# Performance work log

Measured on AMD Instinct MI355X. Metric: run time of the kernel, lower is better.

## Reference

```python
import jax, jax.numpy as jnp
import numpy as np

NUM_PHRASE = 8
HDIM = 256
NUM_HEADS = 8
NUM_LAYERS = 3
MIN_DIST = 2


def sine_pos(mask, num_feats, temperature=10000.0):
    # PositionEmbeddingSine (1D, DETR-style, normalize=False)
    B, L = mask.shape
    x_embed = jnp.cumsum(mask.astype(jnp.float32), axis=1)            # [B,L]
    dim_t = jnp.arange(num_feats, dtype=jnp.float32)
    dim_t = temperature ** (2.0 * jnp.floor(dim_t / 2.0) / num_feats)
    pos = x_embed[:, :, None] / dim_t                                  # [B,L,C]
    pos = jnp.stack([jnp.sin(pos[:, :, 0::2]), jnp.cos(pos[:, :, 1::2])], axis=3)
    return pos.reshape(B, L, num_feats)


def layer_norm(x, g, b, eps=1e-5):
    mu = jnp.mean(x, axis=-1, keepdims=True)
    var = jnp.mean((x - mu) ** 2, axis=-1, keepdims=True)
    return (x - mu) / jnp.sqrt(var + eps) * g + b


def mha(q, k, v, key_mask, in_w, in_b, out_w, out_b, nheads):
    # torch nn.MultiheadAttention (batch_first, eval/no-dropout), averaged attn weights
    B, Lq, C = q.shape
    Dh = C // nheads
    qp = (q @ in_w[:, :C] + in_b[:C]).reshape(B, Lq, nheads, Dh)
    kp = (k @ in_w[:, C:2 * C] + in_b[C:2 * C]).reshape(B, -1, nheads, Dh)
    vp = (v @ in_w[:, 2 * C:] + in_b[2 * C:]).reshape(B, -1, nheads, Dh)
    scores = jnp.einsum('bqhd,bkhd->bhqk', qp, kp) / jnp.sqrt(jnp.float32(Dh))
    scores = jnp.where(key_mask[:, None, None, :], scores, -jnp.inf)
    attn = jax.nn.softmax(scores, axis=-1)
    out = jnp.einsum('bhqk,bkhd->bqhd', attn, vp).reshape(B, Lq, C)
    return out @ out_w + out_b, jnp.mean(attn, axis=1)


def cross_attention(x, y, mask, qw, qb, kvw, kvb, inw, inb, ow, ob, g0, b0, lw, lb, g1, b1):
    C = x.shape[-1]
    q = x @ qw + qb
    kv = y @ kvw + kvb
    k, v = kv[..., :C], kv[..., C:]
    q_att, attn = mha(q, k, v, mask, inw, inb, ow, ob, NUM_HEADS)
    x = layer_norm(x + q_att, g0, b0)
    update = jax.nn.relu(x @ lw + lb)
    x = layer_norm(x + update, g1, b1)
    return x, attn


def _select_one(entropy_b, mask_b):
    # greedy highest-entropy selection with min-distance suppression (1D NMS)
    P, MD = NUM_PHRASE, MIN_DIST
    score = jnp.where(mask_b, entropy_b, -jnp.inf)
    order = jnp.argsort(-score).astype(jnp.int32)   # valid indices first, descending entropy

    def step(carry, idx):
        sel, cnt = carry
        dists = jnp.where(sel >= 0, jnp.abs(idx - sel), 1000000)
        ok = mask_b[idx] & (cnt < P) & (jnp.min(dists) >= MD)
        new_sel = jnp.where(ok, sel.at[jnp.minimum(cnt, P - 1)].set(idx), sel)
        return (new_sel, cnt + ok.astype(jnp.int32)), None

    init = (jnp.full((P,), -1, jnp.int32), jnp.int32(0))
    (sel, cnt), _ = jax.lax.scan(step, init, order)
    last = sel[jnp.maximum(cnt - 1, 0)]
    return jnp.where(jnp.arange(P) < cnt, sel, last)   # pad by repeating last


def phrase_generate(txt_emb, txt_mask, video_feats, video_mask,
                    word_proj_w, word_proj_b, video_proj_w, video_proj_b,
                    q_w, q_b, kv_w, kv_b, in_w, in_b, out_w, out_b,
                    ln0_g, ln0_b, lin_w, lin_b, ln1_g, ln1_b, eos_slot):
    B, L, C = txt_emb.shape
    word_emb = txt_emb[:, 1:]
    word_mask = txt_mask[:, 1:]
    word_pe = word_emb + sine_pos(word_mask, C)

    # word importance via video cross-attention entropy
    wp = word_pe @ word_proj_w + word_proj_b                      # [B,Lw,C]
    vp = video_feats @ video_proj_w + video_proj_b                # [B,T,C]
    sim = jnp.einsum('blc,btc->blt', wp, vp)                      # [B,Lw,T]
    sim = jnp.where(video_mask[:, None, :], sim, -jnp.inf)
    attn_weights = jax.nn.softmax(sim, axis=2)
    entropy = -jnp.sum(attn_weights * jnp.log(attn_weights + 1e-6), axis=2)  # [B,Lw]

    sel = jax.vmap(_select_one)(entropy, word_mask)               # [B,P] int32
    phrase_slot = jnp.take_along_axis(word_pe, sel[:, :, None], axis=1)      # [B,P,C]

    slot_sim = None
    for i in range(NUM_LAYERS):
        phrase_slot, slot_sim = cross_attention(
            phrase_slot, word_pe, word_mask,
            q_w[i], q_b[i], kv_w[i], kv_b[i], in_w[i], in_b[i], out_w[i], out_b[i],
            ln0_g[i], ln0_b[i], lin_w[i], lin_b[i], ln1_g[i], ln1_b[i])

    eos = jnp.broadcast_to(eos_slot, (B, 1, C))
    return phrase_slot, attn_weights, slot_sim, eos


def setup_inputs() -> dict:
    key = jax.random.key(0)
    ks = jax.random.split(key, 16)
    B, L, T, C, NL = 128, 257, 1024, HDIM, NUM_LAYERS
    s = 0.02
    inp = {
        'txt_emb': jax.random.normal(ks[0], (B, L, C), jnp.float32),
        'txt_mask': jnp.ones((B, L), jnp.bool_),
        'video_feats': jax.random.normal(ks[1], (B, T, C), jnp.float32),
        'video_mask': jnp.ones((B, T), jnp.bool_),
        'word_proj_w': jax.random.normal(ks[2], (C, C)) * s,
        'word_proj_b': jnp.zeros((C,)),
        'video_proj_w': jax.random.normal(ks[3], (C, C)) * s,
        'video_proj_b': jnp.zeros((C,)),
        'q_w': jax.random.normal(ks[4], (NL, C, C)) * s,
        'q_b': jnp.zeros((NL, C)),
        'kv_w': jax.random.normal(ks[5], (NL, C, 2 * C)) * s,
        'kv_b': jnp.zeros((NL, 2 * C)),
        'in_w': jax.random.normal(ks[6], (NL, C, 3 * C)) * s,
        'in_b': jnp.zeros((NL, 3 * C)),
        'out_w': jax.random.normal(ks[7], (NL, C, C)) * s,
        'out_b': jnp.zeros((NL, C)),
        'ln0_g': jnp.ones((NL, C)),
        'ln0_b': jnp.zeros((NL, C)),
        'lin_w': jax.random.normal(ks[8], (NL, C, C)) * s,
        'lin_b': jnp.zeros((NL, C)),
        'ln1_g': jnp.ones((NL, C)),
        'ln1_b': jnp.zeros((NL, C)),
        'eos_slot': jax.random.normal(ks[9], (1, 1, C)),
    }
    return inp


def reference(txt_emb, txt_mask, video_feats, video_mask,
              word_proj_w, word_proj_b, video_proj_w, video_proj_b,
              q_w, q_b, kv_w, kv_b, in_w, in_b, out_w, out_b,
              ln0_g, ln0_b, lin_w, lin_b, ln1_g, ln1_b, eos_slot):
    return phrase_generate(txt_emb, txt_mask, video_feats, video_mask,
                           word_proj_w, word_proj_b, video_proj_w, video_proj_b,
                           q_w, q_b, kv_w, kv_b, in_w, in_b, out_w, out_b,
                           ln0_g, ln0_b, lin_w, lin_b, ln1_g, ln1_b, eos_slot)
```

## Files before the change

kernel.cpp:

```cpp
#include <hip/hip_runtime.h>
#include <math.h>

#define BB 128
#define LFULL 257
#define LW 256
#define TT 1024
#define CC 256
#define NH 8
#define DHD 32
#define PP 8
#define NLAY 3

typedef __bf16 bf16x8 __attribute__((ext_vector_type(8)));
typedef __bf16 bf16x4 __attribute__((ext_vector_type(4)));
typedef float  f32x4  __attribute__((ext_vector_type(4)));

__device__ __forceinline__ float blockReduceSum(float v, volatile float* lds) {
#pragma unroll
    for (int m = 32; m >= 1; m >>= 1) v += __shfl_xor(v, m);
    __syncthreads();
    if ((threadIdx.x & 63) == 0) lds[threadIdx.x >> 6] = v;
    __syncthreads();
    return lds[0] + lds[1] + lds[2] + lds[3];
}
__device__ __forceinline__ float blockReduceMax(float v, volatile float* lds) {
#pragma unroll
    for (int m = 32; m >= 1; m >>= 1) v = fmaxf(v, __shfl_xor(v, m));
    __syncthreads();
    if ((threadIdx.x & 63) == 0) lds[threadIdx.x >> 6] = v;
    __syncthreads();
    return fmaxf(fmaxf(lds[0], lds[1]), fmaxf(lds[2], lds[3]));
}


__device__ __forceinline__ int ldsoff(int row, int col) {
    return ((row >> 6) << 11)
         + ((((row >> 4) & 3) << 2) + (col >> 3)) * 128
         + ((row & 15) << 3) + (col & 7);
}

template<int SPLIT, int B_F32, int OUT_SPLIT>
__global__ __launch_bounds__(512, 4) void gemm_mfma(
    const __bf16* __restrict__ Ahi, const __bf16* __restrict__ Alo, int lda, long long sA,
    const void* __restrict__ Bhp, const void* __restrict__ Blp, int ldb, long long sB,
    const float* __restrict__ bias,
    float* __restrict__ Cf, __bf16* __restrict__ Chi, __bf16* __restrict__ Clo,
    int ldc, long long sC, int M, int N, int K)
{
    __shared__ __bf16 sAh[2][4096];
    __shared__ __bf16 sAl[SPLIT ? 2 : 1][SPLIT ? 4096 : 1];
    __shared__ __bf16 sBh[2][4096];
    __shared__ __bf16 sBl[SPLIT ? 2 : 1][SPLIT ? 4096 : 1];

    const int tid = threadIdx.x;
    const int n0 = blockIdx.x * 128;
    const int m0 = blockIdx.y * 128;
    const long long bz = blockIdx.z;
    const __bf16* Ah = Ahi + bz * sA;
    const __bf16* Al = SPLIT ? (Alo + bz * sA) : nullptr;

    const int wv = tid >> 6, lane = tid & 63;
    const int wm = (wv & 1) << 6;
    const int wn = (wv >> 1) << 5;
    const int lr = lane & 15, quad = lane >> 4;

    const int sr = tid >> 2;
    const int sc = (tid & 3) << 3;
    const int soff = ldsoff(sr, sc);
    const long long aoff = (long long)(m0 + sr) * lda + sc;
    const long long boff = (long long)(n0 + sr) * ldb + sc;

    const int abase = ((wm >> 6) << 11) + (lane << 3);
    const int bbase = ((wn >> 6) << 11) + (((wn >> 4) & 3) << 9) + (lane << 3);

    bf16x8 rAh, rAl, rBh, rBl;
    float4 rB0, rB1;

    auto LOADREGS = [&](int k0) {
        rAh = *(const bf16x8*)&Ah[aoff + k0];
        if constexpr (SPLIT) rAl = *(const bf16x8*)&Al[aoff + k0];
        if constexpr (B_F32) {
            const float* Bf = (const float*)Bhp + bz * sB;
            rB0 = *(const float4*)&Bf[boff + k0];
            rB1 = *(const float4*)&Bf[boff + k0 + 4];
        } else {
            const __bf16* Bh = (const __bf16*)Bhp + bz * sB;
            rBh = *(const bf16x8*)&Bh[boff + k0];
            if constexpr (SPLIT) {
                const __bf16* Bl = (const __bf16*)Blp + bz * sB;
                rBl = *(const bf16x8*)&Bl[boff + k0];
            }
        }
    };
    auto WRITELDS = [&](int buf) {
        *(bf16x8*)&sAh[buf][soff] = rAh;
        if constexpr (SPLIT) *(bf16x8*)&sAl[buf][soff] = rAl;
        if constexpr (B_F32) {
            bf16x8 h8, l8;
            h8[0] = (__bf16)rB0.x; l8[0] = (__bf16)(rB0.x - (float)h8[0]);
            h8[1] = (__bf16)rB0.y; l8[1] = (__bf16)(rB0.y - (float)h8[1]);
            h8[2] = (__bf16)rB0.z; l8[2] = (__bf16)(rB0.z - (float)h8[2]);
            h8[3] = (__bf16)rB0.w; l8[3] = (__bf16)(rB0.w - (float)h8[3]);
            h8[4] = (__bf16)rB1.x; l8[4] = (__bf16)(rB1.x - (float)h8[4]);
            h8[5] = (__bf16)rB1.y; l8[5] = (__bf16)(rB1.y - (float)h8[5]);
            h8[6] = (__bf16)rB1.z; l8[6] = (__bf16)(rB1.z - (float)h8[6]);
            h8[7] = (__bf16)rB1.w; l8[7] = (__bf16)(rB1.w - (float)h8[7]);
            *(bf16x8*)&sBh[buf][soff] = h8;
            *(bf16x8*)&sBl[buf][soff] = l8;
        } else {
            *(bf16x8*)&sBh[buf][soff] = rBh;
            if constexpr (SPLIT) *(bf16x8*)&sBl[buf][soff] = rBl;
        }
    };

    f32x4 acc[4][2];
#pragma unroll
    for (int i = 0; i < 4; ++i)
#pragma unroll
        for (int j = 0; j < 2; ++j) acc[i][j] = (f32x4)(0.f);

    const int nt = K >> 5;
    LOADREGS(0);
    WRITELDS(0);
    int cur = 0;
    for (int t = 0; t < nt; ++t) {
        __syncthreads();
        if (t + 1 < nt) LOADREGS((t + 1) << 5);

        bf16x8 fah[4], fbh[2];
        bf16x8 fal[4], fbl[2];
#pragma unroll
        for (int i = 0; i < 4; ++i) {
            fah[i] = *(const bf16x8*)&sAh[cur][abase + i * 512];
            if constexpr (SPLIT)
                fal[i] = *(const bf16x8*)&sAl[cur][abase + i * 512];
        }
#pragma unroll
        for (int j = 0; j < 2; ++j) {
            fbh[j] = *(const bf16x8*)&sBh[cur][bbase + j * 512];
            if constexpr (SPLIT)
                fbl[j] = *(const bf16x8*)&sBl[cur][bbase + j * 512];
        }
#pragma unroll
        for (int i = 0; i < 4; ++i)
#pragma unroll
            for (int j = 0; j < 2; ++j) {
                if constexpr (SPLIT) {
                    acc[i][j] = __builtin_amdgcn_mfma_f32_16x16x32_bf16(fal[i], fbh[j], acc[i][j], 0, 0, 0);
                    acc[i][j] = __builtin_amdgcn_mfma_f32_16x16x32_bf16(fah[i], fbl[j], acc[i][j], 0, 0, 0);
                }
                acc[i][j] = __builtin_amdgcn_mfma_f32_16x16x32_bf16(fah[i], fbh[j], acc[i][j], 0, 0, 0);
            }

        if (t + 1 < nt) WRITELDS(cur ^ 1);
        cur ^= 1;
    }

#pragma unroll
    for (int i = 0; i < 4; ++i)
#pragma unroll
        for (int j = 0; j < 2; ++j) {
            int col = n0 + wn + j * 16 + lr;
            int row0 = m0 + wm + i * 16 + quad * 4;
            float bv = bias ? bias[col] : 0.f;
#pragma unroll
            for (int r = 0; r < 4; ++r) {
                float v = acc[i][j][r] + bv;
                long long off = (long long)(row0 + r) * ldc + col + bz * sC;
                if constexpr (OUT_SPLIT) {
                    __bf16 h = (__bf16)v;
                    Chi[off] = h;
                    Clo[off] = (__bf16)(v - (float)h);
                } else {
                    Cf[off] = v;
                }
            }
        }
}

#define GTS 64
#define GKT 16
#define GPAD 68

template<int TRANSB, int RELU, int TRANSC>
__global__ __launch_bounds__(256) void gemm_f32(
    const float* __restrict__ A, int lda, long long sA,
    const float* __restrict__ Bm, int ldb, long long sB,
    const float* __restrict__ bias,
    float* __restrict__ C, int ldc, long long sC,
    int M, int N, int K)
{
    __shared__ float As[GKT][GPAD];
    __shared__ float Bs[GKT][GPAD];
    const int tid = threadIdx.x;
    const int tx = tid & 15, ty = tid >> 4;
    const int n0 = blockIdx.x * GTS;
    const int m0 = blockIdx.y * GTS;
    const long long bz = blockIdx.z;
    const float* Ab = A + bz * sA;
    const float* Bb = Bm + bz * sB;
    float* Cb = C + bz * sC;

    const int lr = tid >> 2;
    const int lc = (tid & 3) << 2;
    const int br = tid >> 4;
    const int bc = (tid & 15) << 2;

    float acc[4][4] = {};

    for (int k0 = 0; k0 < K; k0 += GKT) {
        float4 a = *(const float4*)&Ab[(long long)(m0 + lr) * lda + k0 + lc];
        As[lc + 0][lr] = a.x; As[lc + 1][lr] = a.y;
        As[lc + 2][lr] = a.z; As[lc + 3][lr] = a.w;
        if (TRANSB) {
            float4 b = *(const float4*)&Bb[(long long)(n0 + lr) * ldb + k0 + lc];
            Bs[lc + 0][lr] = b.x; Bs[lc + 1][lr] = b.y;
            Bs[lc + 2][lr] = b.z; Bs[lc + 3][lr] = b.w;
        } else {
            float4 b = *(const float4*)&Bb[(long long)(k0 + br) * ldb + n0 + bc];
            *(float4*)&Bs[br][bc] = b;
        }
        __syncthreads();
#pragma unroll
        for (int k = 0; k < GKT; ++k) {
            float4 av = *(const float4*)&As[k][ty << 2];
            float4 bv = *(const float4*)&Bs[k][tx << 2];
            float ar[4] = {av.x, av.y, av.z, av.w};
            float brr[4] = {bv.x, bv.y, bv.z, bv.w};
#pragma unroll
            for (int i = 0; i < 4; ++i)
#pragma unroll
                for (int j = 0; j < 4; ++j)
                    acc[i][j] = fmaf(ar[i], brr[j], acc[i][j]);
        }
        __syncthreads();
    }

    float bbr[4] = {0.f, 0.f, 0.f, 0.f};
    if (bias) {
        float4 bb = *(const float4*)&bias[n0 + (tx << 2)];
        bbr[0] = bb.x; bbr[1] = bb.y; bbr[2] = bb.z; bbr[3] = bb.w;
    }
#pragma unroll
    for (int i = 0; i < 4; ++i) {
#pragma unroll
        for (int j = 0; j < 4; ++j) {
            float o = acc[i][j] + bbr[j];
            if (RELU) o = fmaxf(o, 0.f);
            if (TRANSC)
                Cb[(long long)(n0 + (tx << 2) + j) * ldc + m0 + (ty << 2) + i] = o;
            else
                Cb[(long long)(m0 + (ty << 2) + i) * ldc + n0 + (tx << 2) + j] = o;
        }
    }
}


__global__ __launch_bounds__(256) void cumsum_kernel(
    const int* __restrict__ tm, int* __restrict__ cums)
{
    int b = blockIdx.x, c = threadIdx.x;
    int lane = c & 63;
    int v = (tm[(long long)b * LFULL + 1 + c] != 0) ? 1 : 0;
#pragma unroll
    for (int off = 1; off < 64; off <<= 1) {
        int t = __shfl_up(v, off);
        if (lane >= off) v += t;
    }
    __shared__ int wsum[4];
    if (lane == 63) wsum[c >> 6] = v;
    __syncthreads();
    int w = c >> 6, add = 0;
    for (int i = 0; i < w; ++i) add += wsum[i];
    cums[b * LW + c] = v + add;
}

__global__ __launch_bounds__(256) void pe_table_kernel(float* __restrict__ petab)
{
    int n = blockIdx.x;
    int c = threadIdx.x;
    int i2 = c & ~1;
    float freq = powf(10000.0f, (float)i2 / (float)CC);
    float arg = (float)n / freq;
    petab[n * CC + c] = (c & 1) ? cosf(arg) : sinf(arg);
}

__global__ __launch_bounds__(256) void word_pe2_kernel(
    const float* __restrict__ te, const int* __restrict__ cums,
    const float* __restrict__ petab,
    __bf16* __restrict__ whi, __bf16* __restrict__ wlo)
{
    int g = blockIdx.x * 256 + threadIdx.x;
    int c0 = (g & 63) << 2;
    int l  = (g >> 6) & 255;
    int b  = g >> 14;
    int cnt = cums[b * LW + l];
    float4 s = *(const float4*)&te[((long long)(b * LFULL + 1 + l)) * CC + c0];
    float4 p = *(const float4*)&petab[cnt * CC + c0];
    float v0 = s.x + p.x, v1 = s.y + p.y, v2 = s.z + p.z, v3 = s.w + p.w;
    bf16x4 h, lo;
    h[0] = (__bf16)v0; lo[0] = (__bf16)(v0 - (float)h[0]);
    h[1] = (__bf16)v1; lo[1] = (__bf16)(v1 - (float)h[1]);
    h[2] = (__bf16)v2; lo[2] = (__bf16)(v2 - (float)h[2]);
    h[3] = (__bf16)v3; lo[3] = (__bf16)(v3 - (float)h[3]);
    long long o = ((long long)(b * LW + l)) * CC + c0;
    *(bf16x4*)&whi[o] = h;
    *(bf16x4*)&wlo[o] = lo;
}

__global__ __launch_bounds__(256) void split_transpose_kernel(
    const float* __restrict__ W, __bf16* __restrict__ hi, __bf16* __restrict__ lo)
{
    int n = blockIdx.x, k = threadIdx.x;
    float v = W[(long long)k * CC + n];
    __bf16 h = (__bf16)v;
    hi[(long long)n * CC + k] = h;
    lo[(long long)n * CC + k] = (__bf16)(v - (float)h);
}
__global__ __launch_bounds__(256) void split_plain_kernel(
    const float* __restrict__ W, __bf16* __restrict__ hi, __bf16* __restrict__ lo)
{
    int g = blockIdx.x * 256 + threadIdx.x;
    float v = W[g];
    __bf16 h = (__bf16)v;
    hi[g] = h;
    lo[g] = (__bf16)(v - (float)h);
}
__global__ __launch_bounds__(256) void cvt_bf16_kernel(
    const float* __restrict__ src, __bf16* __restrict__ dst)
{
    int g = blockIdx.x * 256 + threadIdx.x;
    dst[g] = (__bf16)src[g];
}

__global__ __launch_bounds__(256) void softmax_entropy_kernel(
    float* __restrict__ attn, const int* __restrict__ vmask,
    float* __restrict__ ent)
{
    __shared__ float lds[4];
    long long row = blockIdx.x;
    int b = blockIdx.x >> 8;
    float* p = attn + row * TT;
    const int* m = vmask + (long long)b * TT;
    int t4 = threadIdx.x * 4;
    float4 v = *(const float4*)&p[t4];
    int4 mm4 = *(const int4*)&m[t4];
    float x[4];
    x[0] = mm4.x ? v.x : -INFINITY;
    x[1] = mm4.y ? v.y : -INFINITY;
    x[2] = mm4.z ? v.z : -INFINITY;
    x[3] = mm4.w ? v.w : -INFINITY;
    float mx = fmaxf(fmaxf(x[0], x[1]), fmaxf(x[2], x[3]));
    mx = blockReduceMax(mx, lds);
    float e[4];
    float ps = 0.f;
#pragma unroll
    for (int j = 0; j < 4; ++j) { e[j] = expf(x[j] - mx); ps += e[j]; }
    float sum = blockReduceSum(ps, lds);
    float q[4];
    float ce = 0.f;
#pragma unroll
    for (int j = 0; j < 4; ++j) {
        q[j] = e[j] / sum;
        ce += q[j] * logf(q[j] + 1e-6f);
    }
    ce = blockReduceSum(ce, lds);
    *(float4*)&p[t4] = make_float4(q[0], q[1], q[2], q[3]);
    if (threadIdx.x == 0) ent[row] = -ce;
}

__global__ __launch_bounds__(256) void select_kernel(
    const float* __restrict__ ent, const int* __restrict__ tm,
    int* __restrict__ sel)
{
    int b = blockIdx.x;
    int l = threadIdx.x;
    __shared__ float sc[LW];
    __shared__ int ord[LW];
    __shared__ unsigned char mk[LW];
    mk[l] = (tm[(long long)b * LFULL + 1 + l] != 0);
    sc[l] = mk[l] ? ent[(long long)b * LW + l] : -INFINITY;
    __syncthreads();
    float mys = sc[l];
    int r = 0;
    for (int j = 0; j < LW; ++j) {
        float s = sc[j];
        r += (s > mys) || (s == mys && j < l);
    }
    ord[r] = l;
    __syncthreads();
    if (l == 0) {
        int chosen[PP];
        int cnt = 0;
        for (int t = 0; t < LW; ++t) {
            int idx = ord[t];
            if (!mk[idx]) continue;
            if (cnt >= PP) break;
            bool ok = true;
            for (int s2 = 0; s2 < cnt; ++s2) {
                int d = idx - chosen[s2];
                if (d < 0) d = -d;
                if (d < 2) ok = false;
            }
            if (ok) chosen[cnt++] = idx;
        }
        int last = (cnt > 0) ? chosen[cnt - 1] : -1;
        for (int p = 0; p < PP; ++p)
            sel[b * PP + p] = (p < cnt) ? chosen[p] : last;
    }
}

__global__ __launch_bounds__(256) void gather_kernel(
    const __bf16* __restrict__ whi, const __bf16* __restrict__ wlo,
    const int* __restrict__ sel, float* __restrict__ x0)
{
    int g = blockIdx.x * 256 + threadIdx.x;
    int b = g >> 11;
    int p = (g >> 8) & 7;
    int c = g & 255;
    int idx = sel[b * PP + p];
    if (idx < 0) idx = 0;
    long long off = ((long long)b * LW + idx) * CC + c;
    x0[g] = (float)whi[off] + (float)wlo[off];
}

__global__ __launch_bounds__(256) void eff_bias_kernel(
    const float* __restrict__ q_b, const float* __restrict__ kv_b,
    const float* __restrict__ in_w, const float* __restrict__ in_b,
    float* __restrict__ BQE_all, float* __restrict__ bkv3)
{
    int i = blockIdx.x / 3;
    int role = blockIdx.x % 3;
    int n = threadIdx.x;
    const float* inw = in_w + (long long)i * 196608;
    const float* inb = in_b + (long long)i * 768;
    const float* srcb;
    int co;
    float* dst;
    if (role == 0)      { srcb = q_b + i * 256;        co = 0;   dst = BQE_all + i * 256; }
    else if (role == 1) { srcb = kv_b + i * 512;       co = 256; dst = bkv3 + i * 512; }
    else                { srcb = kv_b + i * 512 + 256; co = 512; dst = bkv3 + i * 512 + 256; }
    float s = inb[co + n];
    for (int k = 0; k < CC; ++k)
        s = fmaf(srcb[k], inw[(long long)k * 768 + co + n], s);
    dst[n] = s;
}

__global__ __launch_bounds__(256) void attn_scores_kernel(
    const float* __restrict__ qp, const float* __restrict__ KV,
    const int* __restrict__ tm, float* __restrict__ attn)
{
    int b = blockIdx.x, h = blockIdx.y;
    int tid = threadIdx.x;
    __shared__ float qs[PP][DHD];
    __shared__ float sc[PP][LW];
    __shared__ float mxs[PP], sms[PP];
    {
        int q = tid >> 5, d = tid & 31;
        qs[q][d] = qp[((long long)(b * PP + q)) * CC + h * DHD + d];
    }
    __syncthreads();
    const float* kr = KV + ((long long)(b * LW + tid)) * 512 + h * DHD;
    float kreg[DHD];
#pragma unroll
    for (int j = 0; j < 8; ++j) {
        float4 f = *(const float4*)&kr[j * 4];
        kreg[j * 4 + 0] = f.x; kreg[j * 4 + 1] = f.y;
        kreg[j * 4 + 2] = f.z; kreg[j * 4 + 3] = f.w;
    }
    bool mk = tm[(long long)b * LFULL + 1 + tid] != 0;
#pragma unroll
    for (int q = 0; q < PP; ++q) {
        float s = 0.f;
#pragma unroll
        for (int d = 0; d < DHD; ++d) s = fmaf(qs[q][d], kreg[d], s);
        sc[q][tid] = mk ? s * 0.17677669529663687f : -INFINITY;
    }
    __syncthreads();
    {
        int q = tid >> 5, j = tid & 31;
        float m = -INFINITY;
        for (int kk = j; kk < LW; kk += 32) m = fmaxf(m, sc[q][kk]);
#pragma unroll
        for (int mm = 16; mm >= 1; mm >>= 1) m = fmaxf(m, __shfl_xor(m, mm, 32));
        float s = 0.f;
        for (int kk = j; kk < LW; kk += 32) s += expf(sc[q][kk] - m);
#pragma unroll
        for (int mm = 16; mm >= 1; mm >>= 1) s += __shfl_xor(s, mm, 32);
        if (j == 0) { mxs[q] = m; sms[q] = s; }
    }
    __syncthreads();
#pragma unroll
    for (int q = 0; q < PP; ++q) {
        float pv = expf(sc[q][tid] - mxs[q]) / sms[q];
        attn[(((long long)(b * NH + h)) * PP + q) * LW + tid] = pv;
    }
}

__global__ __launch_bounds__(256) void attn_out_kernel(
    const float* __restrict__ attn, const float* __restrict__ KV,
    float* __restrict__ aout)
{
    int b = blockIdx.x, q = blockIdx.y;
    int c = threadIdx.x, h = c >> 5;
    __shared__ float att[NH][LW];
#pragma unroll
    for (int hh = 0; hh < NH; ++hh)
        att[hh][c] = attn[(((long long)(b * NH + hh)) * PP + q) * LW + c];
    __syncthreads();
    const float* vpb = KV + ((long long)b * LW) * 512 + 256 + c;
    float acc = 0.f;
#pragma unroll 8
    for (int k = 0; k < LW; ++k)
        acc = fmaf(att[h][k], vpb[(long long)k * 512], acc);
    aout[((long long)(b * PP + q)) * CC + c] = acc;
}

__global__ __launch_bounds__(256) void slot_sim_kernel(
    const float* __restrict__ attn, float* __restrict__ outs)
{
    int b = blockIdx.x, q = blockIdx.y, k = threadIdx.x;
    float s = 0.f;
#pragma unroll
    for (int h = 0; h < NH; ++h)
        s += attn[(((long long)(b * NH + h)) * PP + q) * LW + k];
    outs[((long long)(b * PP + q)) * LW + k] = s * 0.125f;
}

__global__ __launch_bounds__(256) void ln_residual_kernel(
    const float* __restrict__ xin, const float* __restrict__ add,
    const float* __restrict__ g, const float* __restrict__ bta,
    float* __restrict__ out)
{
    __shared__ float lds[4];
    int r = blockIdx.x, c = threadIdx.x;
    long long idx = (long long)r * CC + c;
    float v = xin[idx] + add[idx];
    float s = blockReduceSum(v, lds);
    float mu = s * (1.0f / (float)CC);
    float d = v - mu;
    float var = blockReduceSum(d * d, lds) * (1.0f / (float)CC);
    out[idx] = d / sqrtf(var + 1e-5f) * g[c] + bta[c];
}

__global__ __launch_bounds__(256) void eos_kernel(
    const float* __restrict__ eos, float* __restrict__ outp)
{
    outp[(long long)blockIdx.x * CC + threadIdx.x] = eos[threadIdx.x];
}

extern "C" void kernel_launch(void* const* d_in, const int* in_sizes, int n_in,
                              void* d_out, int out_size, void* d_ws, size_t ws_size,
                              hipStream_t stream) {
    const float* txt_emb     = (const float*)d_in[0];
    const int*   txt_mask    = (const int*)d_in[1];
    const float* video_feats = (const float*)d_in[2];
    const int*   video_mask  = (const int*)d_in[3];
    const float* word_proj_w = (const float*)d_in[4];
    const float* word_proj_b = (const float*)d_in[5];
    const float* video_proj_w = (const float*)d_in[6];
    const float* q_w   = (const float*)d_in[8];
    const float* q_b   = (const float*)d_in[9];
    const float* kv_w  = (const float*)d_in[10];
    const float* kv_b  = (const float*)d_in[11];
    const float* in_w  = (const float*)d_in[12];
    const float* in_b  = (const float*)d_in[13];
    const float* out_w = (const float*)d_in[14];
    const float* out_b = (const float*)d_in[15];
    const float* ln0_g = (const float*)d_in[16];
    const float* ln0_b = (const float*)d_in[17];
    const float* lin_w = (const float*)d_in[18];
    const float* lin_b = (const float*)d_in[19];
    const float* ln1_g = (const float*)d_in[20];
    const float* ln1_b = (const float*)d_in[21];
    const float* eos_slot = (const float*)d_in[22];

    float* ws = (float*)d_ws;
    __bf16* wpe_hi = (__bf16*)(ws + 0LL);
    __bf16* wpe_lo = (__bf16*)(ws + 4194304LL);
    __bf16* wp_hi  = (__bf16*)(ws + 8388608LL);
    __bf16* wp_lo  = (__bf16*)(ws + 12582912LL);
    __bf16* U_hi   = (__bf16*)(ws + 16777216LL);
    __bf16* U_lo   = (__bf16*)(ws + 20971520LL);
    float*  KV     = ws + 8388608LL;
    float* ent     = ws + 25165824LL;
    int*   sel     = (int*)(ws + 25198592LL);
    float* x0      = ws + 25199616LL;
    float* x1      = ws + 25461760LL;
    float* xmid    = ws + 25723904LL;
    float* qp      = ws + 25986048LL;
    float* attnw   = ws + 26248192LL;
    float* aout    = ws + 28345344LL;
    float* qatt    = ws + 28607488LL;
    float* upd     = ws + 28869632LL;
    float* WQE_all = ws + 29131776LL;
    float* BQE_all = ws + 29328384LL;
    float* WT3f    = ws + 29329152LL;
    __bf16* WT3    = (__bf16*)(ws + 29722368LL);
    float* bkv3    = ws + 29918976LL;
    __bf16* WPT_hi = (__bf16*)(ws + 29920512LL);
    __bf16* WPT_lo = (__bf16*)(ws + 29953280LL);
    __bf16* VPS_hi = (__bf16*)(ws + 29986048LL);
    __bf16* VPS_lo = (__bf16*)(ws + 30018816LL);

    int*   cums  = (int*)(ws + 8388608LL);
    float* petab = ws + 8421376LL;

    float* outp     = (float*)d_out;
    float* out_ps   = outp;
    float* out_attn = outp + 262144LL;
    float* out_slot = outp + 33816576LL;
    float* out_eos  = outp + 34078720LL;

    cumsum_kernel<<<dim3(BB), dim3(256), 0, stream>>>(txt_mask, cums);
    pe_table_kernel<<<dim3(257), dim3(256), 0, stream>>>(petab);
    word_pe2_kernel<<<dim3(8192), dim3(256), 0, stream>>>(txt_emb, cums, petab, wpe_hi, wpe_lo);
    split_transpose_kernel<<<dim3(256), dim3(256), 0, stream>>>(word_proj_w, WPT_hi, WPT_lo);
    split_plain_kernel<<<dim3(256), dim3(256), 0, stream>>>(video_proj_w, VPS_hi, VPS_lo);
    gemm_mfma<1,0,1><<<dim3(2,256,1), dim3(512), 0, stream>>>(
        wpe_hi, wpe_lo, 256, 0, WPT_hi, WPT_lo, 256, 0, word_proj_b,
        nullptr, wp_hi, wp_lo, 256, 0, 32768, 256, 256);
    gemm_mfma<1,0,1><<<dim3(2,256,1), dim3(512), 0, stream>>>(
        wp_hi, wp_lo, 256, 0, VPS_hi, VPS_lo, 256, 0, nullptr,
        nullptr, U_hi, U_lo, 256, 0, 32768, 256, 256);
    gemm_mfma<1,1,0><<<dim3(8,2,BB), dim3(512), 0, stream>>>(
        U_hi, U_lo, 256, 65536LL, video_feats, nullptr, 256, 262144LL, nullptr,
        out_attn, nullptr, nullptr, 1024, 262144LL, 256, 1024, 256);
    softmax_entropy_kernel<<<dim3(32768), dim3(256), 0, stream>>>(out_attn, video_mask, ent);
    select_kernel<<<dim3(BB), dim3(256), 0, stream>>>(ent, txt_mask, sel);
    gather_kernel<<<dim3(1024), dim3(256), 0, stream>>>(wpe_hi, wpe_lo, sel, x0);

    gemm_f32<0,0,0><<<dim3(4,4,3), dim3(256), 0, stream>>>(
        q_w,256,65536LL, in_w,768,196608LL, nullptr, WQE_all,256,65536LL, 256,256,256);
    gemm_f32<0,0,1><<<dim3(4,4,3), dim3(256), 0, stream>>>(
        kv_w,512,131072LL, in_w+256,768,196608LL, nullptr, WT3f,256,131072LL, 256,256,256);
    gemm_f32<0,0,1><<<dim3(4,4,3), dim3(256), 0, stream>>>(
        kv_w+256,512,131072LL, in_w+512,768,196608LL, nullptr, WT3f+65536,256,131072LL, 256,256,256);
    eff_bias_kernel<<<dim3(9), dim3(256), 0, stream>>>(q_b, kv_b, in_w, in_b, BQE_all, bkv3);
    cvt_bf16_kernel<<<dim3(1536), dim3(256), 0, stream>>>(WT3f, (__bf16*)WT3);

    float* X = x0;
    for (int i = 0; i < NLAY; ++i) {
        const float* ow  = out_w + (long long)i * 65536;
        const float* ob  = out_b + (long long)i * 256;
        const float* g0  = ln0_g + (long long)i * 256;
        const float* b0  = ln0_b + (long long)i * 256;
        const float* lw  = lin_w + (long long)i * 65536;
        const float* lb  = lin_b + (long long)i * 256;
        const float* g1  = ln1_g + (long long)i * 256;
        const float* b1  = ln1_b + (long long)i * 256;

        gemm_mfma<0,0,0><<<dim3(4,256,1), dim3(512), 0, stream>>>(
            wpe_hi, nullptr, 256, 0, WT3 + (long long)i * 131072, nullptr, 256, 0,
            bkv3 + i * 512, KV, nullptr, nullptr, 512, 0, 32768, 512, 256);

        gemm_f32<0,0,0><<<dim3(4,16,1), dim3(256), 0, stream>>>(
            X,256,0, WQE_all + (long long)i*65536,256,0, BQE_all + i*256, qp,256,0, 1024,256,256);

        attn_scores_kernel<<<dim3(BB,NH), dim3(256), 0, stream>>>(qp, KV, txt_mask, attnw);
        attn_out_kernel<<<dim3(BB,PP), dim3(256), 0, stream>>>(attnw, KV, aout);
        if (i == NLAY - 1)
            slot_sim_kernel<<<dim3(BB,PP), dim3(256), 0, stream>>>(attnw, out_slot);

        gemm_f32<0,0,0><<<dim3(4,16,1), dim3(256), 0, stream>>>(
            aout,256,0, ow,256,0, ob, qatt,256,0, 1024,256,256);
        ln_residual_kernel<<<dim3(1024), dim3(256), 0, stream>>>(X, qatt, g0, b0, xmid);
        gemm_f32<0,1,0><<<dim3(4,16,1), dim3(256), 0, stream>>>(
            xmid,256,0, lw,256,0, lb, upd,256,0, 1024,256,256);
        float* Xout = (i == NLAY - 1) ? out_ps : ((X == x0) ? x1 : x0);
        ln_residual_kernel<<<dim3(1024), dim3(256), 0, stream>>>(xmid, upd, g1, b1, Xout);
        X = Xout;
    }
    eos_kernel<<<dim3(BB), dim3(256), 0, stream>>>(eos_slot, out_eos);
}
```

Before: 890.7 us.

## Deepen GEMM global-load prefetch to two tiles with dual register sets

Rewrites the MFMA GEMM main loop to keep two register staging sets, so global loads are issued two K-tiles ahead instead of one. The loop is unrolled by two with explicit LDS double-buffer indices, and A fragments are loaded per row-block inside the MFMA loop. The intent is to hide more global memory latency behind MFMA work. The cost is higher register pressure, which could lower occupancy. It also adds an unroll-8 pragma to the bias-precompute inner loop.

Measured after the change: 889.9 us. Within noise of the previous version (-0.1%).

```diff
diff --git a/kernel.cpp b/kernel.cpp
--- a/kernel.cpp
+++ b/kernel.cpp
@@ -73,88 +73,101 @@
     const int abase = ((wm >> 6) << 11) + (lane << 3);
     const int bbase = ((wn >> 6) << 11) + (((wn >> 4) & 3) << 9) + (lane << 3);
 
-    bf16x8 rAh, rAl, rBh, rBl;
-    float4 rB0, rB1;
-
-    auto LOADREGS = [&](int k0) {
-        rAh = *(const bf16x8*)&Ah[aoff + k0];
-        if constexpr (SPLIT) rAl = *(const bf16x8*)&Al[aoff + k0];
-        if constexpr (B_F32) {
-            const float* Bf = (const float*)Bhp + bz * sB;
-            rB0 = *(const float4*)&Bf[boff + k0];
-            rB1 = *(const float4*)&Bf[boff + k0 + 4];
-        } else {
-            const __bf16* Bh = (const __bf16*)Bhp + bz * sB;
-            rBh = *(const bf16x8*)&Bh[boff + k0];
+    bf16x8 rAh0, rAl0, rBh0, rBl0; float4 rBa0, rBb0;
+    bf16x8 rAh1, rAl1, rBh1, rBl1; float4 rBa1, rBb1;
+
+#define LOADR(S, k0) do {                                                         \
+    rAh##S = *(const bf16x8*)&Ah[aoff + (k0)];                                    \
+    if constexpr (SPLIT) rAl##S = *(const bf16x8*)&Al[aoff + (k0)];               \
+    if constexpr (B_F32) {                                                        \
+        const float* Bf_ = (const float*)Bhp + bz * sB;                           \
+        rBa##S = *(const float4*)&Bf_[boff + (k0)];                               \
+        rBb##S = *(const float4*)&Bf_[boff + (k0) + 4];                           \
+    } else {                                                                      \
+        const __bf16* Bh_ = (const __bf16*)Bhp + bz * sB;                         \
+        rBh##S = *(const bf16x8*)&Bh_[boff + (k0)];                               \
+        if constexpr (SPLIT) {                                                    \
+            const __bf16* Bl_ = (const __bf16*)Blp + bz * sB;                     \
+            rBl##S = *(const bf16x8*)&Bl_[boff + (k0)];                           \
+        }                                                                         \
+    } } while (0)
+
+#define WRITEL(S, buf) do {                                                       \
+    *(bf16x8*)&sAh[buf][soff] = rAh##S;                                           \
+    if constexpr (SPLIT) *(bf16x8*)&sAl[buf][soff] = rAl##S;                      \
+    if constexpr (B_F32) {                                                        \
+        bf16x8 h8_, l8_;                                                          \
+        h8_[0] = (__bf16)rBa##S.x; l8_[0] = (__bf16)(rBa##S.x - (float)h8_[0]);   \
+        h8_[1] = (__bf16)rBa##S.y; l8_[1] = (__bf16)(rBa##S.y - (float)h8_[1]);   \
+        h8_[2] = (__bf16)rBa##S.z; l8_[2] = (__bf16)(rBa##S.z - (float)h8_[2]);   \
+        h8_[3] = (__bf16)rBa##S.w; l8_[3] = (__bf16)(rBa##S.w - (float)h8_[3]);   \
+        h8_[4] = (__bf16)rBb##S.x; l8_[4] = (__bf16)(rBb##S.x - (float)h8_[4]);   \
+        h8_[5] = (__bf16)rBb##S.y; l8_[5] = (__bf16)(rBb##S.y - (float)h8_[5]);   \
+        h8_[6] = (__bf16)rBb##S.z; l8_[6] = (__bf16)(rBb##S.z - (float)h8_[6]);   \
+        h8_[7] = (__bf16)rBb##S.w; l8_[7] = (__bf16)(rBb##S.w - (float)h8_[7]);   \
+        *(bf16x8*)&sBh[buf][soff] = h8_;                                          \
+        *(bf16x8*)&sBl[buf][soff] = l8_;                                          \
+    } else {                                                                      \
+        *(bf16x8*)&sBh[buf][soff] = rBh##S;                                       \
+        if constexpr (SPLIT) *(bf16x8*)&sBl[buf][soff] = rBl##S;                  \
+    } } while (0)
+
+    f32x4 acc[4][2];
+#pragma unroll
+    for (int i = 0; i < 4; ++i)
+#pragma unroll
+        for (int j = 0; j < 2; ++j) acc[i][j] = (f32x4)(0.f);
+
+    auto DOMFMA = [&](int buf) {
+        bf16x8 fbh[2], fbl[2];
+#pragma unroll
+        for (int j = 0; j < 2; ++j) {
+            fbh[j] = *(const bf16x8*)&sBh[buf][bbase + j * 512];
+            if constexpr (SPLIT)
+                fbl[j] = *(const bf16x8*)&sBl[buf][bbase + j * 512];
+        }
+#pragma unroll
+        for (int i = 0; i < 4; ++i) {
+            bf16x8 fah = *(const bf16x8*)&sAh[buf][abase + i * 512];
             if constexpr (SPLIT) {
-                const __bf16* Bl = (const __bf16*)Blp + bz * sB;
-                rBl = *(const bf16x8*)&Bl[boff + k0];
+                bf16x8 fal = *(const bf16x8*)&sAl[buf][abase + i * 512];
+#pragma unroll
+                for (int j = 0; j < 2; ++j) {
+                    acc[i][j] = __builtin_amdgcn_mfma_f32_16x16x32_bf16(fal, fbh[j], acc[i][j], 0, 0, 0);
+                    acc[i][j] = __builtin_amdgcn_mfma_f32_16x16x32_bf16(fah, fbl[j], acc[i][j], 0, 0, 0);
+                    acc[i][j] = __builtin_amdgcn_mfma_f32_16x16x32_bf16(fah, fbh[j], acc[i][j], 0, 0, 0);
+                }
+            } else {
+#pragma unroll
+                for (int j = 0; j < 2; ++j)
+                    acc[i][j] = __builtin_amdgcn_mfma_f32_16x16x32_bf16(fah, fbh[j], acc[i][j], 0, 0, 0);
             }
         }
     };
-    auto WRITELDS = [&](int buf) {
-        *(bf16x8*)&sAh[buf][soff] = rAh;
-        if constexpr (SPLIT) *(bf16x8*)&sAl[buf][soff] = rAl;
-        if constexpr (B_F32) {
-            bf16x8 h8, l8;
-            h8[0] = (__bf16)rB0.x; l8[0] = (__bf16)(rB0.x - (float)h8[0]);
-            h8[1] = (__bf16)rB0.y; l8[1] = (__bf16)(rB0.y - (float)h8[1]);
-            h8[2] = (__bf16)rB0.z; l8[2] = (__bf16)(rB0.z - (float)h8[2]);
-            h8[3] = (__bf16)rB0.w; l8[3] = (__bf16)(rB0.w - (float)h8[3]);
-            h8[4] = (__bf16)rB1.x; l8[4] = (__bf16)(rB1.x - (float)h8[4]);
-            h8[5] = (__bf16)rB1.y; l8[5] = (__bf16)(rB1.y - (float)h8[5]);
-            h8[6] = (__bf16)rB1.z; l8[6] = (__bf16)(rB1.z - (float)h8[6]);
-            h8[7] = (__bf16)rB1.w; l8[7] = (__bf16)(rB1.w - (float)h8[7]);
-            *(bf16x8*)&sBh[buf][soff] = h8;
-            *(bf16x8*)&sBl[buf][soff] = l8;
-        } else {
-            *(bf16x8*)&sBh[buf][soff] = rBh;
-            if constexpr (SPLIT) *(bf16x8*)&sBl[buf][soff] = rBl;
-        }
-    };
-
-    f32x4 acc[4][2];
-#pragma unroll
-    for (int i = 0; i < 4; ++i)
-#pragma unroll
-        for (int j = 0; j < 2; ++j) acc[i][j] = (f32x4)(0.f);
 
     const int nt = K >> 5;
-    LOADREGS(0);
-    WRITELDS(0);
-    int cur = 0;
-    for (int t = 0; t < nt; ++t) {
-        __syncthreads();
-        if (t + 1 < nt) LOADREGS((t + 1) << 5);
-
-        bf16x8 fah[4], fbh[2];
-        bf16x8 fal[4], fbl[2];
-#pragma unroll
-        for (int i = 0; i < 4; ++i) {
-            fah[i] = *(const bf16x8*)&sAh[cur][abase + i * 512];
-            if constexpr (SPLIT)
-                fal[i] = *(const bf16x8*)&sAl[cur][abase + i * 512];
-        }
-#pragma unroll
-        for (int j = 0; j < 2; ++j) {
-            fbh[j] = *(const bf16x8*)&sBh[cur][bbase + j * 512];
-            if constexpr (SPLIT)
-                fbl[j] = *(const bf16x8*)&sBl[cur][bbase + j * 512];
-        }
-#pragma unroll
-        for (int i = 0; i < 4; ++i)
-#pragma unroll
-            for (int j = 0; j < 2; ++j) {
-                if constexpr (SPLIT) {
-                    acc[i][j] = __builtin_amdgcn_mfma_f32_16x16x32_bf16(fal[i], fbh[j], acc[i][j], 0, 0, 0);
-                    acc[i][j] = __builtin_amdgcn_mfma_f32_16x16x32_bf16(fah[i], fbl[j], acc[i][j], 0, 0, 0);
-                }
-                acc[i][j] = __builtin_amdgcn_mfma_f32_16x16x32_bf16(fah[i], fbh[j], acc[i][j], 0, 0, 0);
+    LOADR(0, 0);
+    if (nt > 1) LOADR(1, 32);
+    WRITEL(0, 0);
+    if (nt > 2) LOADR(0, 64);
+    __syncthreads();
+
+    for (int t = 0; t < nt; t += 2) {
+        DOMFMA(0);
+        if (t + 1 < nt) {
+            WRITEL(1, 1);
+            if (t + 3 < nt) LOADR(1, (t + 3) << 5);
+            __syncthreads();
+            DOMFMA(1);
+            if (t + 2 < nt) {
+                WRITEL(0, 0);
+                if (t + 4 < nt) LOADR(0, (t + 4) << 5);
+                __syncthreads();
             }
-
-        if (t + 1 < nt) WRITELDS(cur ^ 1);
-        cur ^= 1;
-    }
+        }
+    }
+#undef LOADR
+#undef WRITEL
 
 #pragma unroll
     for (int i = 0; i < 4; ++i)
@@ -441,6 +454,7 @@
     else if (role == 1) { srcb = kv_b + i * 512;       co = 256; dst = bkv3 + i * 512; }
     else                { srcb = kv_b + i * 512 + 256; co = 512; dst = bkv3 + i * 512 + 256; }
     float s = inb[co + n];
+#pragma unroll 8
     for (int k = 0; k < CC; ++k)
         s = fmaf(srcb[k], inw[(long long)k * 768 + co + n], s);
     dst[n] = s;
```
